# Performance work log

Hardware: AMD Instinct MI355X
Metric: run time of the kernel (lower is better)

## Reference

```python
import jax, jax.numpy as jnp
import numpy as np

DIM = 2048
HID = 5632  # multiple_of*ceil((2/3*8192)/256)
CONV = 4
SEQ = 8192


def setup_inputs() -> dict:
    key = jax.random.key(0)
    ks = jax.random.split(key, 6)
    x = jax.random.normal(ks[0], (1, SEQ, DIM), dtype=jnp.float32)
    cu_seqlens = jnp.array([0, 2048, 4096, 6144, 8192], dtype=jnp.int32)
    s = DIM ** -0.5
    w_w = jax.random.normal(ks[1], (HID, DIM), dtype=jnp.float32) * s
    wz_w = jax.random.normal(ks[2], (HID, DIM), dtype=jnp.float32) * s
    wh_w = jax.random.normal(ks[3], (HID, DIM), dtype=jnp.float32) * s
    wo_w = jax.random.normal(ks[4], (DIM, HID), dtype=jnp.float32) * (HID ** -0.5)
    conv_w = jax.random.normal(ks[5], (HID, CONV), dtype=jnp.float32) * (CONV ** -0.5)
    return {"x": x, "cu_seqlens": cu_seqlens, "w_w": w_w, "wz_w": wz_w,
            "wh_w": wh_w, "wo_w": wo_w, "conv_w": conv_w}


def _segment_ids(cu_seqlens, seq_len):
    start = jnp.zeros((seq_len,), dtype=jnp.int32).at[cu_seqlens[:-1]].set(1)
    return start, jnp.cumsum(start)  # start marker, segment id per position


def _causal_conv(z, conv_w, seg_id):
    # z: (b, s, H); depthwise causal conv, w[:, -1] multiplies current step,
    # masked so taps never cross cu_seqlens boundaries.
    s = z.shape[1]
    out = z * conv_w[:, CONV - 1][None, None, :]
    for k in range(1, CONV):
        zs = jnp.pad(z, ((0, 0), (k, 0), (0, 0)))[:, :s]
        sid = jnp.pad(seg_id, (k, 0))[:s]
        valid = (sid == seg_id) & (jnp.arange(s) >= k)
        out = out + zs * conv_w[:, CONV - 1 - k][None, None, :] * valid[None, :, None].astype(z.dtype)
    return out


def _linear_scan(a, b):
    # h_t = a_t * h_{t-1} + b_t along axis=1, via parallel associative scan
    def combine(l, r):
        al, bl = l
        ar, br = r
        return ar * al, ar * bl + br
    _, h = jax.lax.associative_scan(combine, (a, b), axis=1)
    return h


def reference(x, cu_seqlens, w_w, wz_w, wh_w, wo_w, conv_w):
    bsz, seq_len, _ = x.shape
    w0 = jnp.einsum('bsd,hd->bsh', x, w_w)
    z = jnp.einsum('bsd,hd->bsh', x, wz_w)
    tilde_h = jnp.einsum('bsd,hd->bsh', x, wh_w)
    start, seg_id = _segment_ids(cu_seqlens, seq_len)
    z = jax.nn.sigmoid(_causal_conv(z, conv_w, seg_id))
    a = (1.0 - z) * (1 - start)[None, :, None].astype(z.dtype)  # reset state at seq starts
    b = z * tilde_h
    h = _linear_scan(a, b)
    h = h * jax.nn.silu(w0)
    return jnp.einsum('bsh,dh->bsd', h, wo_w)
```

## Files before the change

### kernel.cpp

```cpp
#include <hip/hip_runtime.h>
#include <stdint.h>

#define DIM 2048
#define HID 5632
#define SEQ 8192
#define NW3 (3*HID)
#define CONV 4
#define CHUNK 64
#define PLDC 8448

typedef __attribute__((ext_vector_type(8))) __bf16 bf16x8;
typedef __attribute__((ext_vector_type(4))) float f32x4;
typedef __attribute__((ext_vector_type(4))) uint16_t u16x4;

__device__ __forceinline__ uint16_t f2bf(float f) {
  union { float f; uint32_t u; } v; v.f = f;
  return (uint16_t)((v.u + 0x7FFFu + ((v.u >> 16) & 1u)) >> 16);
}
__device__ __forceinline__ float bf2f(uint16_t h) {
  union { uint32_t u; float f; } v; v.u = ((uint32_t)h) << 16;
  return v.f;
}

__global__ void cvt4_kernel(const float* __restrict__ src, uint16_t* __restrict__ dst, int n4) {
  int i = blockIdx.x * blockDim.x + threadIdx.x;
  if (i >= n4) return;
  float4 v = ((const float4*)src)[i];
  ushort4 o;
  o.x = f2bf(v.x); o.y = f2bf(v.y); o.z = f2bf(v.z); o.w = f2bf(v.w);
  ((ushort4*)dst)[i] = o;
}

__device__ __forceinline__ void load_lds16(const void* g, void* l) {
  __builtin_amdgcn_global_load_lds(
      (__attribute__((address_space(1))) void*)g,
      (__attribute__((address_space(3))) void*)l, 16, 0, 0);
}

template<int LDA, int LDB, int LDC, int LDC2, int KLEN, int OUT_MODE>
__global__ __launch_bounds__(512, 4)
void gemm128(const uint16_t* __restrict__ A, const uint16_t* __restrict__ B,
             void* __restrict__ C, float* __restrict__ C2, int nbx)
{
  __shared__ alignas(16) uint16_t As[3][128][32];
  __shared__ alignas(16) uint16_t Bs[3][256][32];
  constexpr int NT = KLEN / 32;

  const int tid  = threadIdx.x;
  const int wave = tid >> 6;
  const int lane = tid & 63;

  const int nwg = (int)gridDim.x;
  const int bid = (int)blockIdx.x;
  const int qq  = nwg >> 3, rr = nwg & 7;
  const int xcd = bid & 7, loc = bid >> 3;
  const int swz = (xcd < rr ? xcd*(qq+1) : rr*(qq+1) + (xcd-rr)*qq) + loc;
  const int row0 = (swz % nbx) * 128;
  const int col0 = (swz / nbx) * 256;

  const uint16_t* Ab = A + (size_t)blockIdx.z * KLEN;
  const uint16_t* Bb = B + (size_t)blockIdx.z * KLEN;

  const int wr = wave >> 2;
  const int wc = wave & 3;
  const int rm = lane & 15;
  const int kq8 = ((lane >> 4) ^ ((rm >> 1) & 3)) * 8;
  const int ri = wr*64 + rm;
  const int ci = wc*64 + rm;

  size_t offA, offB0, offB1;
  {
    const int ra = tid >> 2,        ka = (tid & 3) ^ ((ra >> 1) & 3);
    const int rb0 = tid >> 2,       kb0 = (tid & 3) ^ ((rb0 >> 1) & 3);
    const int g1 = 512 + tid;
    const int rb1 = g1 >> 2,        kb1 = (g1 & 3) ^ ((rb1 >> 1) & 3);
    offA  = (size_t)(row0 + ra)*LDA + ka*8;
    offB0 = (size_t)(col0 + rb0)*LDB + kb0*8;
    offB1 = (size_t)(col0 + rb1)*LDB + kb1*8;
  }

#define STAGE(kt,buf) do {                                                  \
    const size_t ko_ = (size_t)(kt)*32;                                     \
    load_lds16(Ab + offA  + ko_, &As[(buf)][wave*16][0]);                   \
    load_lds16(Bb + offB0 + ko_, &Bs[(buf)][wave*16][0]);                   \
    load_lds16(Bb + offB1 + ko_, &Bs[(buf)][128 + wave*16][0]);             \
  } while (0)
#define PIN() __builtin_amdgcn_sched_barrier(0)

  f32x4 acc[4][4];
  #pragma unroll
  for (int i = 0; i < 4; ++i)
    #pragma unroll
    for (int j = 0; j < 4; ++j) acc[i][j] = (f32x4){0.f,0.f,0.f,0.f};

  STAGE(0, 0);
  {
    const int t1 = (NT > 1) ? 1 : 0;
    STAGE(t1, 1);
  }
  asm volatile("s_waitcnt vmcnt(3)" ::: "memory");
  __builtin_amdgcn_s_barrier();
  PIN();

  int c = 0;
  #pragma unroll 1
  for (int t = 0; t < NT; ++t) {
    const int tn2 = (t+2 < NT) ? t+2 : NT-1;
    int cs = c + 2; if (cs >= 3) cs -= 3;

    bf16x8 af[4], bfr[4];
    #pragma unroll
    for (int i = 0; i < 4; ++i) af[i]  = *(const bf16x8*)&As[c][ri + i*16][kq8];
    #pragma unroll
    for (int j = 0; j < 4; ++j) bfr[j] = *(const bf16x8*)&Bs[c][ci + j*16][kq8];
    STAGE(tn2, cs);
    PIN();
    asm volatile("s_waitcnt lgkmcnt(0)" ::: "memory");
    PIN();
    __builtin_amdgcn_s_setprio(1);
    #pragma unroll
    for (int i = 0; i < 4; ++i)
      #pragma unroll
      for (int j = 0; j < 4; ++j)
        acc[i][j] = __builtin_amdgcn_mfma_f32_16x16x32_bf16(af[i], bfr[j], acc[i][j], 0, 0, 0);
    __builtin_amdgcn_s_setprio(0);
    asm volatile("s_waitcnt vmcnt(3)" ::: "memory");
    __builtin_amdgcn_s_barrier();
    PIN();

    c += 1; if (c >= 3) c = 0;
  }
#undef STAGE
#undef PIN

  const int cr = (lane >> 4) * 4;
  const int cc = lane & 15;
  #pragma unroll
  for (int i = 0; i < 4; ++i)
    #pragma unroll
    for (int j = 0; j < 4; ++j) {
      const int r_ = row0 + wr*64 + i*16 + cr;
      const int c_ = col0 + wc*64 + j*16 + cc;
      #pragma unroll
      for (int r = 0; r < 4; ++r) {
        const float v = acc[i][j][r];
        if (OUT_MODE == 1) {
          ((uint16_t*)C)[(size_t)(r_ + r)*LDC + c_] = f2bf(v);
        } else if (OUT_MODE == 2) {
          if (blockIdx.z == 0) C2[(size_t)(r_ + r)*LDC2 + c_] = v;
          else                 ((float*)C)[(size_t)(r_ + r)*LDC + c_] = v;
        } else {
          ((float*)C)[(size_t)(r_ + r)*LDC + c_] = v;
        }
      }
    }
}

__global__ void addP_kernel(float* __restrict__ out, const float* __restrict__ P, int n4) {
  int i = blockIdx.x * blockDim.x + threadIdx.x;
  if (i >= n4) return;
  int r  = i >> 9;
  int c4 = i & 511;
  float4 a = ((float4*)out)[i];
  float4 b = *(const float4*)&P[(size_t)r*PLDC + c4*4];
  a.x += b.x; a.y += b.y; a.z += b.z; a.w += b.w;
  ((float4*)out)[i] = a;
}


__device__ __forceinline__ void seg_info(const int* cuv, int ns, int t, int& ss, bool& st) {
  ss = 0; st = false;
  for (int i=0;i<ns;i++) { int cv = cuv[i]; if (cv<=t && cv>ss) ss=cv; if (cv==t) st=true; }
}

__global__ void scan_chunk(const uint16_t* __restrict__ G, int qstart,
                           const uint16_t* __restrict__ zprev,
                           const float* __restrict__ convw,
                           const int* __restrict__ cu, int ncu,
                           float* __restrict__ Ach, float* __restrict__ Bch)
{
  const int h0 = (blockIdx.x * blockDim.x + threadIdx.x) * 4;
  const int c  = blockIdx.y;
  const uint16_t* Z  = G + HID;
  const uint16_t* TH = G + 2*HID;
  float4 wv[4];
  #pragma unroll
  for (int j=0;j<4;j++) wv[j] = ((const float4*)convw)[h0+j];
  int cuv[8];
  int ns = ncu - 1; if (ns > 8) ns = 8;
  for (int i=0;i<ns;i++) cuv[i] = cu[i];
  const int r0 = c * CHUNK;
  const int t0 = qstart + r0;
  float z1[4], z2[4], z3[4];
  if (c == 0) {
    u16x4 a1 = *(const u16x4*)&zprev[2*HID + h0];
    u16x4 a2 = *(const u16x4*)&zprev[1*HID + h0];
    u16x4 a3 = *(const u16x4*)&zprev[0*HID + h0];
    #pragma unroll
    for (int j=0;j<4;j++) {
      z1[j] = (t0-1 >= 0) ? bf2f(a1[j]) : 0.f;
      z2[j] = (t0-2 >= 0) ? bf2f(a2[j]) : 0.f;
      z3[j] = (t0-3 >= 0) ? bf2f(a3[j]) : 0.f;
    }
  } else {
    u16x4 a1 = *(const u16x4*)&Z[(size_t)(r0-1)*NW3 + h0];
    u16x4 a2 = *(const u16x4*)&Z[(size_t)(r0-2)*NW3 + h0];
    u16x4 a3 = *(const u16x4*)&Z[(size_t)(r0-3)*NW3 + h0];
    #pragma unroll
    for (int j=0;j<4;j++) { z1[j]=bf2f(a1[j]); z2[j]=bf2f(a2[j]); z3[j]=bf2f(a3[j]); }
  }
  float Aacc[4] = {1.f,1.f,1.f,1.f};
  float Bacc[4] = {0.f,0.f,0.f,0.f};
  u16x4 zv = *(const u16x4*)&Z[(size_t)r0*NW3 + h0];
  u16x4 tv = *(const u16x4*)&TH[(size_t)r0*NW3 + h0];
  for (int r = r0; r < r0 + CHUNK; ++r) {
    const int rn = (r+1 < r0+CHUNK) ? r+1 : r;
    u16x4 zn = *(const u16x4*)&Z[(size_t)rn*NW3 + h0];
    u16x4 tn = *(const u16x4*)&TH[(size_t)rn*NW3 + h0];
    const int t = qstart + r;
    int ss; bool st;
    seg_info(cuv, ns, t, ss, st);
    const bool k1 = (t-1 >= ss), k2 = (t-2 >= ss), k3 = (t-3 >= ss);
    #pragma unroll
    for (int j=0;j<4;j++) {
      const float zc0 = bf2f(zv[j]);
      float s = zc0*wv[j].w;
      if (k1) s += z1[j]*wv[j].z;
      if (k2) s += z2[j]*wv[j].y;
      if (k3) s += z3[j]*wv[j].x;
      const float zc = 1.f/(1.f + __expf(-s));
      const float a = st ? 0.f : (1.f - zc);
      const float b = zc * bf2f(tv[j]);
      Aacc[j] *= a;
      Bacc[j] = a*Bacc[j] + b;
      z3[j] = z2[j]; z2[j] = z1[j]; z1[j] = zc0;
    }
    zv = zn; tv = tn;
  }
  *(float4*)&Ach[(size_t)c*HID + h0] = make_float4(Aacc[0],Aacc[1],Aacc[2],Aacc[3]);
  *(float4*)&Bch[(size_t)c*HID + h0] = make_float4(Bacc[0],Bacc[1],Bacc[2],Bacc[3]);
}

__global__ void scan_combine(float* __restrict__ Ach, const float* __restrict__ Bch,
                             float* __restrict__ Sc, int first, int nchunk)
{
  const int h0 = (blockIdx.x * blockDim.x + threadIdx.x) * 4;
  float4 s;
  if (first) s = make_float4(0.f,0.f,0.f,0.f);
  else       s = *(const float4*)&Sc[h0];
  for (int c = 0; c < nchunk; ++c) {
    const size_t idx = (size_t)c*HID + h0;
    float4 a = *(const float4*)&Ach[idx];
    float4 b = *(const float4*)&Bch[idx];
    *(float4*)&Ach[idx] = s;
    s.x = a.x*s.x + b.x;
    s.y = a.y*s.y + b.y;
    s.z = a.z*s.z + b.z;
    s.w = a.w*s.w + b.w;
  }
  *(float4*)&Sc[h0] = s;
}

__global__ void scan_final(uint16_t* __restrict__ G, int qstart,
                           const uint16_t* __restrict__ zprev,
                           const float* __restrict__ convw,
                           const int* __restrict__ cu, int ncu,
                           const float* __restrict__ Hin)
{
  const int h0 = (blockIdx.x * blockDim.x + threadIdx.x) * 4;
  const int c  = blockIdx.y;
  const uint16_t* W0 = G;
  const uint16_t* Z  = G + HID;
  uint16_t*       TH = G + 2*HID;
  float4 wv[4];
  #pragma unroll
  for (int j=0;j<4;j++) wv[j] = ((const float4*)convw)[h0+j];
  int cuv[8];
  int ns = ncu - 1; if (ns > 8) ns = 8;
  for (int i=0;i<ns;i++) cuv[i] = cu[i];
  const int r0 = c * CHUNK;
  const int t0 = qstart + r0;
  float z1[4], z2[4], z3[4];
  if (c == 0) {
    u16x4 a1 = *(const u16x4*)&zprev[2*HID + h0];
    u16x4 a2 = *(const u16x4*)&zprev[1*HID + h0];
    u16x4 a3 = *(const u16x4*)&zprev[0*HID + h0];
    #pragma unroll
    for (int j=0;j<4;j++) {
      z1[j] = (t0-1 >= 0) ? bf2f(a1[j]) : 0.f;
      z2[j] = (t0-2 >= 0) ? bf2f(a2[j]) : 0.f;
      z3[j] = (t0-3 >= 0) ? bf2f(a3[j]) : 0.f;
    }
  } else {
    u16x4 a1 = *(const u16x4*)&Z[(size_t)(r0-1)*NW3 + h0];
    u16x4 a2 = *(const u16x4*)&Z[(size_t)(r0-2)*NW3 + h0];
    u16x4 a3 = *(const u16x4*)&Z[(size_t)(r0-3)*NW3 + h0];
    #pragma unroll
    for (int j=0;j<4;j++) { z1[j]=bf2f(a1[j]); z2[j]=bf2f(a2[j]); z3[j]=bf2f(a3[j]); }
  }
  float state[4];
  {
    float4 hv = *(const float4*)&Hin[(size_t)c*HID + h0];
    state[0]=hv.x; state[1]=hv.y; state[2]=hv.z; state[3]=hv.w;
  }
  u16x4 zv = *(const u16x4*)&Z[(size_t)r0*NW3 + h0];
  u16x4 tv = *(const u16x4*)&TH[(size_t)r0*NW3 + h0];
  u16x4 wvv = *(const u16x4*)&W0[(size_t)r0*NW3 + h0];
  for (int r = r0; r < r0 + CHUNK; ++r) {
    const int rn = (r+1 < r0+CHUNK) ? r+1 : r;
    u16x4 zn = *(const u16x4*)&Z[(size_t)rn*NW3 + h0];
    u16x4 tn = *(const u16x4*)&TH[(size_t)rn*NW3 + h0];
    u16x4 wn = *(const u16x4*)&W0[(size_t)rn*NW3 + h0];
    const int t = qstart + r;
    int ss; bool st;
    seg_info(cuv, ns, t, ss, st);
    const bool k1 = (t-1 >= ss), k2 = (t-2 >= ss), k3 = (t-3 >= ss);
    u16x4 outv;
    #pragma unroll
    for (int j=0;j<4;j++) {
      const float zc0 = bf2f(zv[j]);
      float s = zc0*wv[j].w;
      if (k1) s += z1[j]*wv[j].z;
      if (k2) s += z2[j]*wv[j].y;
      if (k3) s += z3[j]*wv[j].x;
      const float zc = 1.f/(1.f + __expf(-s));
      const float a = st ? 0.f : (1.f - zc);
      const float b = zc * bf2f(tv[j]);
      state[j] = a*state[j] + b;
      const float w0v = bf2f(wvv[j]);
      const float silu = w0v / (1.f + __expf(-w0v));
      outv[j] = f2bf(state[j] * silu);
      z3[j] = z2[j]; z2[j] = z1[j]; z1[j] = zc0;
    }
    *(u16x4*)&TH[(size_t)r*NW3 + h0] = outv;
    zv = zn; tv = tn; wvv = wn;
  }
}

__global__ void save_ztail(const uint16_t* __restrict__ G, uint16_t* __restrict__ zprev, int qrows) {
  int i4 = (blockIdx.x * blockDim.x + threadIdx.x) * 4;
  if (i4 >= 3*HID) return;
  int j = i4 / HID;
  int h = i4 - j*HID;
  *(u16x4*)&zprev[i4] = *(const u16x4*)&G[(size_t)(qrows-3+j)*NW3 + HID + h];
}

extern "C" void kernel_launch(void* const* d_in, const int* in_sizes, int n_in,
                              void* d_out, int out_size, void* d_ws, size_t ws_size,
                              hipStream_t stream) {
  const float* x     = (const float*)d_in[0];
  const int*   cu    = (const int*)d_in[1];
  const float* w_w   = (const float*)d_in[2];
  const float* wz_w  = (const float*)d_in[3];
  const float* wh_w  = (const float*)d_in[4];
  const float* wo_w  = (const float*)d_in[5];
  const float* convw = (const float*)d_in[6];
  const int ncu = in_sizes[1];
  float* out = (float*)d_out;

  const size_t base = 92331008ull;
  int qrows = 2048;
  if (ws_size >= base + 8192ull*38592ull) qrows = 8192;
  else if (ws_size >= base + 4096ull*38592ull) qrows = 4096;
  const int nq = SEQ / qrows;
  const int nchunk = qrows / CHUNK;

  char* p = (char*)d_ws;
  uint16_t* w3b  = (uint16_t*)p; p += (size_t)NW3*DIM*2;
  uint16_t* wob  = (uint16_t*)p; p += (size_t)DIM*HID*2;
  float*    Sc   = (float*)p;    p += (size_t)HID*4;
  uint16_t* zprev= (uint16_t*)p; p += (size_t)3*HID*2;
  uint16_t* xseg = (uint16_t*)p; p += (size_t)qrows*DIM*2;
  uint16_t* G    = (uint16_t*)p; p += (size_t)qrows*NW3*2;
  float*    Ach  = (float*)p;    p += (size_t)nchunk*HID*4;
  float*    Bch  = (float*)p;    p += (size_t)nchunk*HID*4;

  {
    int n4 = HID*DIM/4;
    cvt4_kernel<<<(n4+255)/256, 256, 0, stream>>>(w_w,  w3b, n4);
    cvt4_kernel<<<(n4+255)/256, 256, 0, stream>>>(wz_w, w3b + (size_t)HID*DIM, n4);
    cvt4_kernel<<<(n4+255)/256, 256, 0, stream>>>(wh_w, w3b + (size_t)2*HID*DIM, n4);
    n4 = DIM*HID/4;
    cvt4_kernel<<<(n4+255)/256, 256, 0, stream>>>(wo_w, wob, n4);
  }

  for (int s = 0; s < nq; ++s) {
    const int qstart = s * qrows;

    int n4 = qrows*DIM/4;
    cvt4_kernel<<<(n4+255)/256, 256, 0, stream>>>(x + (size_t)qstart*DIM, xseg, n4);

    {
      const int nbx = qrows / 128;
      gemm128<DIM, DIM, NW3, 0, DIM, 1><<<dim3(nbx * (NW3/256), 1, 1), 512, 0, stream>>>(
          xseg, w3b, G, nullptr, nbx);
    }

    scan_chunk  <<<dim3(11, nchunk), 128, 0, stream>>>(G, qstart, zprev, convw, cu, ncu, Ach, Bch);
    scan_combine<<<11, 128, 0, stream>>>(Ach, Bch, Sc, s == 0 ? 1 : 0, nchunk);
    scan_final  <<<dim3(11, nchunk), 128, 0, stream>>>(G, qstart, zprev, convw, cu, ncu, Ach);

    if (s + 1 < nq)
      save_ztail<<<(3*HID/4+127)/128, 128, 0, stream>>>(G, zprev, qrows);

    const int nbx2 = qrows / 128;
    float* P = (float*)G;
    if (qrows == 8192) {
      gemm128<NW3, HID, DIM, 0, HID, 0><<<dim3(nbx2*(DIM/256), 1, 1), 512, 0, stream>>>(
          G + 2*HID, wob, out + (size_t)qstart*DIM, nullptr, nbx2);
    } else {
      gemm128<NW3, HID, DIM, PLDC, HID/2, 2><<<dim3(nbx2*(DIM/256), 1, 2), 512, 0, stream>>>(
          G + 2*HID, wob, out + (size_t)qstart*DIM, P, nbx2);
      int na = qrows * (DIM/4);
      addP_kernel<<<(na+255)/256, 256, 0, stream>>>(out + (size_t)qstart*DIM, P, na);
    }
  }
}
```

Baseline: 1.385 ms.

## Use 32x32x16 MFMA in GEMM, make scan chunk size runtime, prefetch combine

The GEMM inner loop moves from sixteen 16x16x32 bf16 MFMAs per wave to eight 32x32x16 MFMAs, with new LDS fragment indexing and epilogue mapping. The aim is to cut LDS reads and instruction issue per FLOP. The scan chunk length becomes a runtime parameter, and the workspace sizing now picks chunk 32 when it fits, which doubles the parallel chunks in the scan kernels. The sequential combine kernel also prefetches the next chunk's values so load latency overlaps the recurrence.

```diff
diff --git a/kernel.cpp b/kernel.cpp
--- a/kernel.cpp
+++ b/kernel.cpp
@@ -6,11 +6,11 @@
 #define SEQ 8192
 #define NW3 (3*HID)
 #define CONV 4
-#define CHUNK 64
 #define PLDC 8448
 
 typedef __attribute__((ext_vector_type(8))) __bf16 bf16x8;
 typedef __attribute__((ext_vector_type(4))) float f32x4;
+typedef __attribute__((ext_vector_type(16))) float f32x16;
 typedef __attribute__((ext_vector_type(4))) uint16_t u16x4;
 
 __device__ __forceinline__ uint16_t f2bf(float f) {
@@ -63,10 +63,11 @@
 
   const int wr = wave >> 2;
   const int wc = wave & 3;
-  const int rm = lane & 15;
-  const int kq8 = ((lane >> 4) ^ ((rm >> 1) & 3)) * 8;
-  const int ri = wr*64 + rm;
-  const int ci = wc*64 + rm;
+  const int r32 = lane & 31;
+  const int kg  = lane >> 5;
+  const int sxor = (r32 >> 1) & 3;
+  const int eo0 = ((0*2 + kg) ^ sxor) * 8;
+  const int eo1 = ((1*2 + kg) ^ sxor) * 8;
 
   size_t offA, offB0, offB1;
   {
@@ -87,11 +88,13 @@
   } while (0)
 #define PIN() __builtin_amdgcn_sched_barrier(0)
 
-  f32x4 acc[4][4];
+  f32x16 acc[2][2];
   #pragma unroll
-  for (int i = 0; i < 4; ++i)
-    #pragma unroll
-    for (int j = 0; j < 4; ++j) acc[i][j] = (f32x4){0.f,0.f,0.f,0.f};
+  for (int i = 0; i < 2; ++i)
+    #pragma unroll
+    for (int j = 0; j < 2; ++j)
+      #pragma unroll
+      for (int e = 0; e < 16; ++e) acc[i][j][e] = 0.f;
 
   STAGE(0, 0);
   {
@@ -108,21 +111,29 @@
     const int tn2 = (t+2 < NT) ? t+2 : NT-1;
     int cs = c + 2; if (cs >= 3) cs -= 3;
 
-    bf16x8 af[4], bfr[4];
-    #pragma unroll
-    for (int i = 0; i < 4; ++i) af[i]  = *(const bf16x8*)&As[c][ri + i*16][kq8];
-    #pragma unroll
-    for (int j = 0; j < 4; ++j) bfr[j] = *(const bf16x8*)&Bs[c][ci + j*16][kq8];
+    bf16x8 a0[2], a1[2], b0[2], b1[2];
+    #pragma unroll
+    for (int b = 0; b < 2; ++b) {
+      a0[b] = *(const bf16x8*)&As[c][wr*64 + b*32 + r32][eo0];
+      a1[b] = *(const bf16x8*)&As[c][wr*64 + b*32 + r32][eo1];
+      b0[b] = *(const bf16x8*)&Bs[c][wc*64 + b*32 + r32][eo0];
+      b1[b] = *(const bf16x8*)&Bs[c][wc*64 + b*32 + r32][eo1];
+    }
     STAGE(tn2, cs);
     PIN();
     asm volatile("s_waitcnt lgkmcnt(0)" ::: "memory");
     PIN();
     __builtin_amdgcn_s_setprio(1);
     #pragma unroll
-    for (int i = 0; i < 4; ++i)
+    for (int i = 0; i < 2; ++i)
       #pragma unroll
-      for (int j = 0; j < 4; ++j)
-        acc[i][j] = __builtin_amdgcn_mfma_f32_16x16x32_bf16(af[i], bfr[j], acc[i][j], 0, 0, 0);
+      for (int j = 0; j < 2; ++j)
+        acc[i][j] = __builtin_amdgcn_mfma_f32_32x32x16_bf16(a0[i], b0[j], acc[i][j], 0, 0, 0);
+    #pragma unroll
+    for (int i = 0; i < 2; ++i)
+      #pragma unroll
+      for (int j = 0; j < 2; ++j)
+        acc[i][j] = __builtin_amdgcn_mfma_f32_32x32x16_bf16(a1[i], b1[j], acc[i][j], 0, 0, 0);
     __builtin_amdgcn_s_setprio(0);
     asm volatile("s_waitcnt vmcnt(3)" ::: "memory");
     __builtin_amdgcn_s_barrier();
@@ -133,24 +144,23 @@
 #undef STAGE
 #undef PIN
 
-  const int cr = (lane >> 4) * 4;
-  const int cc = lane & 15;
   #pragma unroll
-  for (int i = 0; i < 4; ++i)
-    #pragma unroll
-    for (int j = 0; j < 4; ++j) {
-      const int r_ = row0 + wr*64 + i*16 + cr;
-      const int c_ = col0 + wc*64 + j*16 + cc;
+  for (int i = 0; i < 2; ++i)
+    #pragma unroll
+    for (int j = 0; j < 2; ++j) {
+      const int rbase = row0 + wr*64 + i*32 + 4*kg;
+      const int c_    = col0 + wc*64 + j*32 + r32;
       #pragma unroll
-      for (int r = 0; r < 4; ++r) {
-        const float v = acc[i][j][r];
+      for (int reg = 0; reg < 16; ++reg) {
+        const int r_ = rbase + (reg & 3) + 8*(reg >> 2);
+        const float v = acc[i][j][reg];
         if (OUT_MODE == 1) {
-          ((uint16_t*)C)[(size_t)(r_ + r)*LDC + c_] = f2bf(v);
+          ((uint16_t*)C)[(size_t)r_*LDC + c_] = f2bf(v);
         } else if (OUT_MODE == 2) {
-          if (blockIdx.z == 0) C2[(size_t)(r_ + r)*LDC2 + c_] = v;
-          else                 ((float*)C)[(size_t)(r_ + r)*LDC + c_] = v;
+          if (blockIdx.z == 0) C2[(size_t)r_*LDC2 + c_] = v;
+          else                 ((float*)C)[(size_t)r_*LDC + c_] = v;
         } else {
-          ((float*)C)[(size_t)(r_ + r)*LDC + c_] = v;
+          ((float*)C)[(size_t)r_*LDC + c_] = v;
         }
       }
     }
@@ -176,7 +186,7 @@
 __global__ void scan_chunk(const uint16_t* __restrict__ G, int qstart,
                            const uint16_t* __restrict__ zprev,
                            const float* __restrict__ convw,
-                           const int* __restrict__ cu, int ncu,
+                           const int* __restrict__ cu, int ncu, int chunk,
                            float* __restrict__ Ach, float* __restrict__ Bch)
 {
   const int h0 = (blockIdx.x * blockDim.x + threadIdx.x) * 4;
@@ -189,7 +199,7 @@
   int cuv[8];
   int ns = ncu - 1; if (ns > 8) ns = 8;
   for (int i=0;i<ns;i++) cuv[i] = cu[i];
-  const int r0 = c * CHUNK;
+  const int r0 = c * chunk;
   const int t0 = qstart + r0;
   float z1[4], z2[4], z3[4];
   if (c == 0) {
@@ -213,8 +223,8 @@
   float Bacc[4] = {0.f,0.f,0.f,0.f};
   u16x4 zv = *(const u16x4*)&Z[(size_t)r0*NW3 + h0];
   u16x4 tv = *(const u16x4*)&TH[(size_t)r0*NW3 + h0];
-  for (int r = r0; r < r0 + CHUNK; ++r) {
-    const int rn = (r+1 < r0+CHUNK) ? r+1 : r;
+  for (int r = r0; r < r0 + chunk; ++r) {
+    const int rn = (r+1 < r0+chunk) ? r+1 : r;
     u16x4 zn = *(const u16x4*)&Z[(size_t)rn*NW3 + h0];
     u16x4 tn = *(const u16x4*)&TH[(size_t)rn*NW3 + h0];
     const int t = qstart + r;
@@ -248,15 +258,18 @@
   float4 s;
   if (first) s = make_float4(0.f,0.f,0.f,0.f);
   else       s = *(const float4*)&Sc[h0];
+  float4 a = *(const float4*)&Ach[h0];
+  float4 b = *(const float4*)&Bch[h0];
   for (int c = 0; c < nchunk; ++c) {
-    const size_t idx = (size_t)c*HID + h0;
-    float4 a = *(const float4*)&Ach[idx];
-    float4 b = *(const float4*)&Bch[idx];
-    *(float4*)&Ach[idx] = s;
+    const int cn = (c+1 < nchunk) ? c+1 : c;
+    float4 an = *(const float4*)&Ach[(size_t)cn*HID + h0];
+    float4 bn = *(const float4*)&Bch[(size_t)cn*HID + h0];
+    *(float4*)&Ach[(size_t)c*HID + h0] = s;
     s.x = a.x*s.x + b.x;
     s.y = a.y*s.y + b.y;
     s.z = a.z*s.z + b.z;
     s.w = a.w*s.w + b.w;
+    a = an; b = bn;
   }
   *(float4*)&Sc[h0] = s;
 }
@@ -264,7 +277,7 @@
 __global__ void scan_final(uint16_t* __restrict__ G, int qstart,
                            const uint16_t* __restrict__ zprev,
                            const float* __restrict__ convw,
-                           const int* __restrict__ cu, int ncu,
+                           const int* __restrict__ cu, int ncu, int chunk,
                            const float* __restrict__ Hin)
 {
   const int h0 = (blockIdx.x * blockDim.x + threadIdx.x) * 4;
@@ -278,7 +291,7 @@
   int cuv[8];
   int ns = ncu - 1; if (ns > 8) ns = 8;
   for (int i=0;i<ns;i++) cuv[i] = cu[i];
-  const int r0 = c * CHUNK;
+  const int r0 = c * chunk;
   const int t0 = qstart + r0;
   float z1[4], z2[4], z3[4];
   if (c == 0) {
@@ -306,8 +319,8 @@
   u16x4 zv = *(const u16x4*)&Z[(size_t)r0*NW3 + h0];
   u16x4 tv = *(const u16x4*)&TH[(size_t)r0*NW3 + h0];
   u16x4 wvv = *(const u16x4*)&W0[(size_t)r0*NW3 + h0];
-  for (int r = r0; r < r0 + CHUNK; ++r) {
-    const int rn = (r+1 < r0+CHUNK) ? r+1 : r;
+  for (int r = r0; r < r0 + chunk; ++r) {
+    const int rn = (r+1 < r0+chunk) ? r+1 : r;
     u16x4 zn = *(const u16x4*)&Z[(size_t)rn*NW3 + h0];
     u16x4 tn = *(const u16x4*)&TH[(size_t)rn*NW3 + h0];
     u16x4 wn = *(const u16x4*)&W0[(size_t)rn*NW3 + h0];
@@ -358,12 +371,19 @@
   const int ncu = in_sizes[1];
   float* out = (float*)d_out;
 
-  const size_t base = 92331008ull;
-  int qrows = 2048;
-  if (ws_size >= base + 8192ull*38592ull) qrows = 8192;
-  else if (ws_size >= base + 4096ull*38592ull) qrows = 4096;
+  auto need = [](long long q, long long ch) -> unsigned long long {
+    return 92331008ull + (unsigned long long)(q*37888ll) +
+           (unsigned long long)((q/ch)*(long long)HID*8ll);
+  };
+  int qrows, chunk;
+  if      (ws_size >= need(8192,32)) { qrows = 8192; chunk = 32; }
+  else if (ws_size >= need(8192,64)) { qrows = 8192; chunk = 64; }
+  else if (ws_size >= need(4096,32)) { qrows = 4096; chunk = 32; }
+  else if (ws_size >= need(4096,64)) { qrows = 4096; chunk = 64; }
+  else if (ws_size >= need(2048,32)) { qrows = 2048; chunk = 32; }
+  else                               { qrows = 2048; chunk = 64; }
   const int nq = SEQ / qrows;
-  const int nchunk = qrows / CHUNK;
+  const int nchunk = qrows / chunk;
 
   char* p = (char*)d_ws;
   uint16_t* w3b  = (uint16_t*)p; p += (size_t)NW3*DIM*2;
@@ -396,9 +416,9 @@
           xseg, w3b, G, nullptr, nbx);
     }
 
-    scan_chunk  <<<dim3(11, nchunk), 128, 0, stream>>>(G, qstart, zprev, convw, cu, ncu, Ach, Bch);
+    scan_chunk  <<<dim3(11, nchunk), 128, 0, stream>>>(G, qstart, zprev, convw, cu, ncu, chunk, Ach, Bch);
     scan_combine<<<11, 128, 0, stream>>>(Ach, Bch, Sc, s == 0 ? 1 : 0, nchunk);
-    scan_final  <<<dim3(11, nchunk), 128, 0, stream>>>(G, qstart, zprev, convw, cu, ncu, Ach);
+    scan_final  <<<dim3(11, nchunk), 128, 0, stream>>>(G, qstart, zprev, convw, cu, ncu, chunk, Ach);
 
     if (s + 1 < nq)
       save_ztail<<<(3*HID/4+127)/128, 128, 0, stream>>>(G, zprev, qrows);
```

Result: slower. 1.467 ms (+5.9%).
